# Performance work log

Measured on AMD Instinct MI355X. Metric: run time of the kernel, lower is better.

Reference implementation:

```python
import jax, jax.numpy as jnp
import numpy as np

B, C, F, D, K = 128, 64, 129, 512, 8192  # batch, channels, stft bins, d_model, codebook size


def setup_inputs() -> dict:
    key = jax.random.key(0)
    k0, k1, k2, k3 = jax.random.split(key, 4)
    x = jax.random.normal(k0, (B, C, F), dtype=jnp.float32)
    # nn.Linear(129, 512): weight stored transposed here as [F, D] for einsum
    W = jax.random.normal(k1, (F, D), dtype=jnp.float32) * (1.0 / np.sqrt(F).astype(np.float32))
    b = jnp.zeros((D,), dtype=jnp.float32)
    codebook = jax.random.normal(k2, (K, D), dtype=jnp.float32)
    pos_emb = jax.random.normal(k3, (1, C, D), dtype=jnp.float32)
    return {"x": x, "W": W, "b": b, "codebook": codebook, "pos_emb": pos_emb}


def reference(x, W, b, codebook, pos_emb):
    # Linear projection: [B,C,F] @ [F,D] -> [B,C,D]
    z = jnp.einsum('bcf,fd->bcd', x, W) + b

    # Vector quantization: nearest codebook entry by squared L2 distance.
    # dist(z,e) = |z|^2 - 2 z.e + |e|^2; argmin unaffected by constant |z|^2 per token,
    # but keep full expression for faithfulness/numerics.
    z2 = jnp.sum(z * z, axis=-1, keepdims=True)              # [B,C,1]
    e2 = jnp.sum(codebook * codebook, axis=-1)               # [K]
    dots = jnp.einsum('bcd,kd->bck', z, codebook)            # [B,C,K] dominant GEMM
    dists = z2 - 2.0 * dots + e2                             # [B,C,K]
    idx = jnp.argmin(dists, axis=-1)                         # [B,C] int
    q = codebook[idx]                                        # gather: [B,C,D]

    # commitment loss: mse(stop_grad(quantize), z)
    commit_loss = jnp.mean(jnp.square(jax.lax.stop_gradient(q) - z))

    # straight-through estimator
    quantized = z + jax.lax.stop_gradient(q - z)

    out = quantized + pos_emb
    return out, commit_loss
```

## Files before the change

kernel.cpp:

```cpp
#include <hip/hip_runtime.h>
#include <hip/hip_bf16.h>
#include <hip/hip_fp16.h>
#include <stdint.h>

#define B_ 128
#define C_ 64
#define F_ 129
#define D_ 512
#define K_ 8192
#define M_ (B_ * C_)

typedef __attribute__((ext_vector_type(8))) _Float16 half8;
typedef __attribute__((ext_vector_type(4))) float f32x4;
typedef unsigned long long u64;

__device__ __forceinline__ ushort f2h(float f) {
  const _Float16 h = (_Float16)f;
  return __builtin_bit_cast(ushort, h);
}

__global__ __launch_bounds__(256) void k_prep(
    const float* __restrict__ x, const float* __restrict__ W,
    const float* __restrict__ bias, const float* __restrict__ cb,
    float* __restrict__ z, ushort* __restrict__ zf, ushort* __restrict__ cf,
    float* __restrict__ e2) {
  const int tid = threadIdx.x;
  if (blockIdx.x < 512) {
    __shared__ float xs[16][F_];
    const int t0 = blockIdx.x * 16;
    const float* xsrc = x + (size_t)t0 * F_;
    for (int i = tid; i < 16 * F_; i += 256) xs[i / F_][i % F_] = xsrc[i];
    __syncthreads();
    float a0[16], a1[16];
#pragma unroll
    for (int r = 0; r < 16; ++r) { a0[r] = 0.f; a1[r] = 0.f; }
    const int c0 = tid, c1 = tid + 256;
    for (int f = 0; f < F_; ++f) {
      const float w0 = W[f * D_ + c0];
      const float w1 = W[f * D_ + c1];
#pragma unroll
      for (int r = 0; r < 16; ++r) {
        const float xv = xs[r][f];
        a0[r] = __builtin_fmaf(xv, w0, a0[r]);
        a1[r] = __builtin_fmaf(xv, w1, a1[r]);
      }
    }
    const float b0 = bias[c0], b1 = bias[c1];
#pragma unroll
    for (int r = 0; r < 16; ++r) {
      const size_t row = (size_t)(t0 + r) * D_;
      const float v0 = a0[r] + b0, v1 = a1[r] + b1;
      z[row + c0] = v0;
      z[row + c1] = v1;
      zf[row + c0] = f2h(v0);
      zf[row + c1] = f2h(v1);
    }
  } else {
    const int row = (blockIdx.x - 512) * 4 + (tid >> 6);
    const int lane = tid & 63;
    const float* src = cb + (size_t)row * D_;
    float s = 0.f;
#pragma unroll
    for (int i = 0; i < 8; ++i) {
      const int d = lane + i * 64;
      const float v = src[d];
      s = __builtin_fmaf(v, v, s);
      cf[(size_t)row * D_ + d] = f2h(v);
    }
#pragma unroll
    for (int o = 32; o > 0; o >>= 1) s += __shfl_down(s, o);
    if (lane == 0) e2[row] = s;
  }
}

__device__ __forceinline__ void stage_tile(const ushort* __restrict__ g,
                                           int r0, int k0, ushort* lds,
                                           int tid) {
  const int c = tid & 7;
#pragma unroll
  for (int i = 0; i < 4; ++i) {
    const int r = i * 32 + (tid >> 3);
    const int cs = c ^ (r & 7);
    const ushort* src = g + (size_t)(r0 + r) * D_ + k0 + cs * 8;
    char* dst = (char*)lds + i * 4096 + (tid >> 6) * 1024;
    __builtin_amdgcn_global_load_lds(
        (const __attribute__((address_space(1))) void*)src,
        (__attribute__((address_space(3))) void*)dst, 16, 0, 0);
  }
}

__device__ __forceinline__ void top2_merge(u64& k1, u64& k2, u64 b1, u64 b2) {
  const u64 m1 = (k1 < b1) ? k1 : b1;
  const u64 hi = (k1 < b1) ? b1 : k1;
  const u64 lo2 = (k2 < b2) ? k2 : b2;
  k2 = (hi < lo2) ? hi : lo2;
  k1 = m1;
}

__global__ __launch_bounds__(256) void k_argmin(
    const ushort* __restrict__ zf, const ushort* __restrict__ cf,
    const float* __restrict__ e2, u64* __restrict__ blk2) {
  __shared__ ushort lA[128 * 64], lB[128 * 64];
  const int tid = threadIdx.x;
  const int lane = tid & 63;
  const int w = tid >> 6;
  const int wr = (w >> 1) * 64;
  const int wc = (w & 1) * 64;
  const int m0 = (blockIdx.x >> 6) * 128;
  const int n0 = (blockIdx.x & 63) * 128;

  f32x4 acc[4][4];
#pragma unroll
  for (int m = 0; m < 4; ++m)
#pragma unroll
    for (int n = 0; n < 4; ++n) acc[m][n] = (f32x4){0.f, 0.f, 0.f, 0.f};

  for (int kt = 0; kt < D_ / 64; ++kt) {
    __syncthreads();
    stage_tile(zf, m0, kt * 64, lA, tid);
    stage_tile(cf, n0, kt * 64, lB, tid);
    asm volatile("s_waitcnt vmcnt(0)" ::: "memory");
    __syncthreads();
#pragma unroll
    for (int ks = 0; ks < 2; ++ks) {
      half8 ah[4], bh[4];
#pragma unroll
      for (int m = 0; m < 4; ++m) {
        const int row = wr + m * 16 + (lane & 15);
        const int cb = (ks * 64 + ((lane >> 4) << 4)) ^ ((row & 7) << 4);
        ah[m] = *(const half8*)((const char*)lA + row * 128 + cb);
      }
#pragma unroll
      for (int n = 0; n < 4; ++n) {
        const int row = wc + n * 16 + (lane & 15);
        const int cb = (ks * 64 + ((lane >> 4) << 4)) ^ ((row & 7) << 4);
        bh[n] = *(const half8*)((const char*)lB + row * 128 + cb);
      }
#pragma unroll
      for (int m = 0; m < 4; ++m)
#pragma unroll
        for (int n = 0; n < 4; ++n)
          acc[m][n] = __builtin_amdgcn_mfma_f32_16x16x32_f16(ah[m], bh[n],
                                                             acc[m][n], 0, 0, 0);
    }
  }

  float e2c[4];
#pragma unroll
  for (int n = 0; n < 4; ++n) e2c[n] = e2[n0 + wc + n * 16 + (lane & 15)];
  const int half = (n0 + wc) >> 6;

#pragma unroll
  for (int m = 0; m < 4; ++m) {
#pragma unroll
    for (int j = 0; j < 4; ++j) {
      u64 k1 = ~0ull, k2 = ~0ull;
#pragma unroll
      for (int n = 0; n < 4; ++n) {
        const float d = __builtin_fmaf(-2.f, acc[m][n][j], e2c[n]);
        uint32_t s = __float_as_uint(d);
        s ^= (s & 0x80000000u) ? 0xFFFFFFFFu : 0x80000000u;
        const u64 c = ((u64)s << 32) |
                      (uint32_t)(n0 + wc + n * 16 + (lane & 15));
        if (c < k1) { k2 = k1; k1 = c; } else if (c < k2) { k2 = c; }
      }
#pragma unroll
      for (int o = 1; o < 16; o <<= 1) {
        const u64 b1 = __shfl_xor(k1, o);
        const u64 b2 = __shfl_xor(k2, o);
        top2_merge(k1, k2, b1, b2);
      }
      if ((lane & 15) == 0) {
        const int row = m0 + wr + m * 16 + (lane >> 4) * 4 + j;
        u64* dst = blk2 + (size_t)row * 256 + half * 2;
        dst[0] = k1;
        dst[1] = k2;
      }
    }
  }
}

#define CS(a, b)                          \
  {                                       \
    const u64 lo_ = (a < b) ? a : b;      \
    const u64 hi_ = (a < b) ? b : a;      \
    a = lo_;                              \
    b = hi_;                              \
  }

__global__ __launch_bounds__(256) void k_resolve(
    const u64* __restrict__ blk2, const float* __restrict__ cb,
    const float* __restrict__ z, const float* __restrict__ pos,
    float* __restrict__ out, float* __restrict__ lossp) {
  const int t = blockIdx.x * 4 + (threadIdx.x >> 6);
  const int lane = threadIdx.x & 63;
  const u64* kp = blk2 + (size_t)t * 256;
  u64 v0 = kp[lane * 4 + 0], v1 = kp[lane * 4 + 1];
  u64 v2 = kp[lane * 4 + 2], v3 = kp[lane * 4 + 3];
  CS(v0, v1) CS(v2, v3) CS(v0, v2) CS(v1, v3) CS(v1, v2)
#pragma unroll
  for (int o = 1; o < 64; o <<= 1) {
    const u64 b0 = __shfl_xor(v0, o), b1 = __shfl_xor(v1, o);
    const u64 b2 = __shfl_xor(v2, o), b3 = __shfl_xor(v3, o);
    u64 m0 = (v0 < b3) ? v0 : b3;
    u64 m1 = (v1 < b2) ? v1 : b2;
    u64 m2 = (v2 < b1) ? v2 : b1;
    u64 m3 = (v3 < b0) ? v3 : b0;
    CS(m0, m2) CS(m1, m3) CS(m0, m1) CS(m2, m3)
    v0 = m0; v1 = m1; v2 = m2; v3 = m3;
  }
  const int i0 = (int)(v0 & 0xFFFFFFFFull);
  const int i1 = (int)(v1 & 0xFFFFFFFFull);
  const int i2 = (int)(v2 & 0xFFFFFFFFull);
  const int i3 = (int)(v3 & 0xFFFFFFFFull);
  const float* c0 = cb + (size_t)i0 * D_;
  const float* c1 = cb + (size_t)i1 * D_;
  const float* c2 = cb + (size_t)i2 * D_;
  const float* c3 = cb + (size_t)i3 * D_;
  const float* zr = z + (size_t)t * D_;
  float zv[8], c0v[8], c1v[8], c2v[8], c3v[8];
  double dt0 = 0.0, dt1 = 0.0, dt2 = 0.0, dt3 = 0.0;
  double q0 = 0.0, q1 = 0.0, q2 = 0.0, q3 = 0.0;
#pragma unroll
  for (int i = 0; i < 8; ++i) {
    const int d = lane + i * 64;
    zv[i] = zr[d];
    c0v[i] = c0[d]; c1v[i] = c1[d]; c2v[i] = c2[d]; c3v[i] = c3[d];
    dt0 += (double)zv[i] * (double)c0v[i]; q0 += (double)c0v[i] * (double)c0v[i];
    dt1 += (double)zv[i] * (double)c1v[i]; q1 += (double)c1v[i] * (double)c1v[i];
    dt2 += (double)zv[i] * (double)c2v[i]; q2 += (double)c2v[i] * (double)c2v[i];
    dt3 += (double)zv[i] * (double)c3v[i]; q3 += (double)c3v[i] * (double)c3v[i];
  }
#pragma unroll
  for (int o = 1; o < 64; o <<= 1) {
    dt0 += __shfl_xor(dt0, o); dt1 += __shfl_xor(dt1, o);
    dt2 += __shfl_xor(dt2, o); dt3 += __shfl_xor(dt3, o);
    q0 += __shfl_xor(q0, o); q1 += __shfl_xor(q1, o);
    q2 += __shfl_xor(q2, o); q3 += __shfl_xor(q3, o);
  }
  const double d0 = q0 - 2.0 * dt0;
  const double d1 = q1 - 2.0 * dt1;
  const double d2 = q2 - 2.0 * dt2;
  const double d3 = q3 - 2.0 * dt3;
  int bsel = 0, bidx = i0;
  double bd = d0;
  if (d1 < bd || (d1 == bd && i1 < bidx)) { bd = d1; bidx = i1; bsel = 1; }
  if (d2 < bd || (d2 == bd && i2 < bidx)) { bd = d2; bidx = i2; bsel = 2; }
  if (d3 < bd || (d3 == bd && i3 < bidx)) { bd = d3; bidx = i3; bsel = 3; }
  const float* pe = pos + (size_t)(t & (C_ - 1)) * D_;
  float part = 0.f;
#pragma unroll
  for (int i = 0; i < 8; ++i) {
    const int d = lane + i * 64;
    const float qv = (bsel == 0) ? c0v[i]
                   : (bsel == 1) ? c1v[i]
                   : (bsel == 2) ? c2v[i] : c3v[i];
    const float df = qv - zv[i];
    part = __builtin_fmaf(df, df, part);
    out[(size_t)t * D_ + d] = qv + pe[d];
  }
#pragma unroll
  for (int o = 32; o > 0; o >>= 1) part += __shfl_down(part, o);
  if (lane == 0) lossp[t] = part;
}

__global__ __launch_bounds__(1024) void k_loss(const float* __restrict__ lossp,
                                               float* __restrict__ loss) {
  const int tid = threadIdx.x;
  float s = 0.f;
  for (int i = tid; i < M_; i += 1024) s += lossp[i];
#pragma unroll
  for (int o = 32; o > 0; o >>= 1) s += __shfl_down(s, o);
  __shared__ float red[16];
  if ((tid & 63) == 0) red[tid >> 6] = s;
  __syncthreads();
  if (tid == 0) {
    float tot = 0.f;
#pragma unroll
    for (int i = 0; i < 16; ++i) tot += red[i];
    *loss = tot * (1.0f / ((float)M_ * (float)D_));
  }
}

extern "C" void kernel_launch(void* const* d_in, const int* in_sizes, int n_in,
                              void* d_out, int out_size, void* d_ws,
                              size_t ws_size, hipStream_t stream) {
  const float* x = (const float*)d_in[0];
  const float* W = (const float*)d_in[1];
  const float* bias = (const float*)d_in[2];
  const float* cb = (const float*)d_in[3];
  const float* pos = (const float*)d_in[4];
  float* out = (float*)d_out;
  float* loss = out + (size_t)M_ * D_;

  char* ws = (char*)d_ws;
  float* z = (float*)(ws + 0);
  ushort* zf = (ushort*)(ws + (16ull << 20));
  ushort* cf = (ushort*)(ws + (24ull << 20));
  float* e2 = (float*)(ws + (32ull << 20));
  float* lossp = (float*)(ws + (32ull << 20) + 32768);
  u64* blk2 = (u64*)(ws + (32ull << 20) + 65536);

  k_prep<<<512 + K_ / 4, 256, 0, stream>>>(x, W, bias, cb, z, zf, cf, e2);
  k_argmin<<<(M_ / 128) * (K_ / 128), 256, 0, stream>>>(zf, cf, e2, blk2);
  k_resolve<<<M_ / 4, 256, 0, stream>>>(blk2, cb, z, pos, out, lossp);
  k_loss<<<1, 1024, 0, stream>>>(lossp, loss);
}
```

Measured before the change: 252.2 us.

## Transpose MFMA operands so argmin reduces codes in-register, fewer cross-lane shuffles

Swaps the A/B operands of the MFMA so each lane's accumulator registers hold several codebook entries for one token. The top-2 search then runs mostly in registers with float/int pairs, and only two xor-shuffle stages are needed instead of four 64-bit shuffle rounds per row. Also adds a launch-bounds occupancy hint of 4 blocks per CU. The epilogue cost is reduced; tie-breaking among equal distances may differ slightly from the packed-key comparison, and the occupancy hint may cause register spills.

Measured after the change: 215.5 us. 1.17x faster.

```diff
diff --git a/kernel.cpp b/kernel.cpp
--- a/kernel.cpp
+++ b/kernel.cpp
@@ -17,6 +17,10 @@
 __device__ __forceinline__ ushort f2h(float f) {
   const _Float16 h = (_Float16)f;
   return __builtin_bit_cast(ushort, h);
+}
+__device__ __forceinline__ uint32_t fmap(float f) {
+  uint32_t s = __float_as_uint(f);
+  return s ^ ((s & 0x80000000u) ? 0xFFFFFFFFu : 0x80000000u);
 }
 
 __global__ __launch_bounds__(256) void k_prep(
@@ -89,15 +93,7 @@
   }
 }
 
-__device__ __forceinline__ void top2_merge(u64& k1, u64& k2, u64 b1, u64 b2) {
-  const u64 m1 = (k1 < b1) ? k1 : b1;
-  const u64 hi = (k1 < b1) ? b1 : k1;
-  const u64 lo2 = (k2 < b2) ? k2 : b2;
-  k2 = (hi < lo2) ? hi : lo2;
-  k1 = m1;
-}
-
-__global__ __launch_bounds__(256) void k_argmin(
+__global__ __launch_bounds__(256, 4) void k_argmin(
     const ushort* __restrict__ zf, const ushort* __restrict__ cf,
     const float* __restrict__ e2, u64* __restrict__ blk2) {
   __shared__ ushort lA[128 * 64], lB[128 * 64];
@@ -123,59 +119,76 @@
     __syncthreads();
 #pragma unroll
     for (int ks = 0; ks < 2; ++ks) {
-      half8 ah[4], bh[4];
+      half8 at[4], bc[4];
 #pragma unroll
       for (int m = 0; m < 4; ++m) {
         const int row = wr + m * 16 + (lane & 15);
-        const int cb = (ks * 64 + ((lane >> 4) << 4)) ^ ((row & 7) << 4);
-        ah[m] = *(const half8*)((const char*)lA + row * 128 + cb);
+        const int cbo = (ks * 64 + ((lane >> 4) << 4)) ^ ((row & 7) << 4);
+        at[m] = *(const half8*)((const char*)lA + row * 128 + cbo);
       }
 #pragma unroll
       for (int n = 0; n < 4; ++n) {
         const int row = wc + n * 16 + (lane & 15);
-        const int cb = (ks * 64 + ((lane >> 4) << 4)) ^ ((row & 7) << 4);
-        bh[n] = *(const half8*)((const char*)lB + row * 128 + cb);
+        const int cbo = (ks * 64 + ((lane >> 4) << 4)) ^ ((row & 7) << 4);
+        bc[n] = *(const half8*)((const char*)lB + row * 128 + cbo);
       }
 #pragma unroll
-      for (int m = 0; m < 4; ++m)
-#pragma unroll
-        for (int n = 0; n < 4; ++n)
-          acc[m][n] = __builtin_amdgcn_mfma_f32_16x16x32_f16(ah[m], bh[n],
-                                                             acc[m][n], 0, 0, 0);
-    }
-  }
-
-  float e2c[4];
-#pragma unroll
-  for (int n = 0; n < 4; ++n) e2c[n] = e2[n0 + wc + n * 16 + (lane & 15)];
+      for (int mc = 0; mc < 4; ++mc)
+#pragma unroll
+        for (int nt = 0; nt < 4; ++nt)
+          acc[mc][nt] = __builtin_amdgcn_mfma_f32_16x16x32_f16(
+              bc[mc], at[nt], acc[mc][nt], 0, 0, 0);
+    }
+  }
+
+  const int cbase = n0 + wc + ((lane >> 4) << 2);
+  float e2r[4][4];
+#pragma unroll
+  for (int mc = 0; mc < 4; ++mc)
+#pragma unroll
+    for (int j = 0; j < 4; ++j) e2r[mc][j] = e2[cbase + mc * 16 + j];
   const int half = (n0 + wc) >> 6;
-
-#pragma unroll
-  for (int m = 0; m < 4; ++m) {
-#pragma unroll
-    for (int j = 0; j < 4; ++j) {
-      u64 k1 = ~0ull, k2 = ~0ull;
-#pragma unroll
-      for (int n = 0; n < 4; ++n) {
-        const float d = __builtin_fmaf(-2.f, acc[m][n][j], e2c[n]);
-        uint32_t s = __float_as_uint(d);
-        s ^= (s & 0x80000000u) ? 0xFFFFFFFFu : 0x80000000u;
-        const u64 c = ((u64)s << 32) |
-                      (uint32_t)(n0 + wc + n * 16 + (lane & 15));
-        if (c < k1) { k2 = k1; k1 = c; } else if (c < k2) { k2 = c; }
+  const int tbase = m0 + wr;
+
+#pragma unroll
+  for (int nt = 0; nt < 4; ++nt) {
+    float v1 = 3.0e38f, v2 = 3.0e38f;
+    int i1 = 0, i2 = 0;
+#pragma unroll
+    for (int mc = 0; mc < 4; ++mc) {
+#pragma unroll
+      for (int j = 0; j < 4; ++j) {
+        const float dd = __builtin_fmaf(-2.f, acc[mc][nt][j], e2r[mc][j]);
+        const int ii = cbase + mc * 16 + j;
+        const bool lt1 = dd < v1;
+        const bool lt2 = dd < v2;
+        v2 = lt1 ? v1 : (lt2 ? dd : v2);
+        i2 = lt1 ? i1 : (lt2 ? ii : i2);
+        v1 = lt1 ? dd : v1;
+        i1 = lt1 ? ii : i1;
       }
-#pragma unroll
-      for (int o = 1; o < 16; o <<= 1) {
-        const u64 b1 = __shfl_xor(k1, o);
-        const u64 b2 = __shfl_xor(k2, o);
-        top2_merge(k1, k2, b1, b2);
-      }
-      if ((lane & 15) == 0) {
-        const int row = m0 + wr + m * 16 + (lane >> 4) * 4 + j;
-        u64* dst = blk2 + (size_t)row * 256 + half * 2;
-        dst[0] = k1;
-        dst[1] = k2;
-      }
+    }
+#pragma unroll
+    for (int o = 16; o < 64; o <<= 1) {
+      const float bv1 = __shfl_xor(v1, o), bv2 = __shfl_xor(v2, o);
+      const int bi1 = __shfl_xor(i1, o), bi2 = __shfl_xor(i2, o);
+      const bool t = bv1 < v1;
+      const float hv = t ? v1 : bv1;
+      const int hi = t ? i1 : bi1;
+      v1 = t ? bv1 : v1;
+      i1 = t ? bi1 : i1;
+      const bool t2 = bv2 < v2;
+      const float cv2 = t2 ? bv2 : v2;
+      const int ci2 = t2 ? bi2 : i2;
+      const bool t3 = hv < cv2;
+      v2 = t3 ? hv : cv2;
+      i2 = t3 ? hi : ci2;
+    }
+    if (lane < 16) {
+      const int row = tbase + nt * 16 + lane;
+      u64* dst = blk2 + (size_t)row * 256 + half * 2;
+      dst[0] = ((u64)fmap(v1) << 32) | (uint32_t)i1;
+      dst[1] = ((u64)fmap(v2) << 32) | (uint32_t)i2;
     }
   }
 }
```
